# Performance work log

Hardware: AMD Instinct MI355X
Metric: run time of the kernel (lower is better)

The kernel has to match this reference:

```python
import jax, jax.numpy as jnp
import numpy as np

N_STATIONS = 276
CONTEXT_LEN = 384  # args.context_len * 2
TARGET_LEN = 96
BATCH = 4096


def setup_inputs() -> dict:
    key = jax.random.key(0)
    k1, k2, k3, k4, k5, k6 = jax.random.split(key, 6)
    z = jax.random.normal(k1, (BATCH, CONTEXT_LEN), dtype=jnp.float32)
    stations = jax.random.randint(k2, (BATCH,), 0, N_STATIONS, dtype=jnp.int64)
    # per-station Linear params (nn.Linear(context_len, target_len) x n_stations)
    lim = 1.0 / np.sqrt(CONTEXT_LEN)
    W = jax.random.uniform(k3, (N_STATIONS, TARGET_LEN, CONTEXT_LEN), jnp.float32, -lim, lim)
    b = jax.random.uniform(k4, (N_STATIONS, TARGET_LEN), jnp.float32, -lim, lim)
    loc = jax.random.normal(k5, (N_STATIONS,), dtype=jnp.float32)
    scale = jax.random.uniform(k6, (N_STATIONS,), jnp.float32, 0.5, 2.0)
    return {"z": z, "stations": stations, "W": W, "b": b, "loc": loc, "scale": scale}


def reference(z, stations, W, b, loc, scale):
    # norm: (z - loc[i]) / scale[i]
    loc_i = loc[stations][:, None]      # (bs, 1)
    scale_i = scale[stations][:, None]  # (bs, 1)
    zn = (z - loc_i) / scale_i          # (bs, context_len)
    # per-sample station-specific Linear: batched GEMV via gathered weights
    out = jnp.einsum("boi,bi->bo", W[stations], zn) + b[stations]  # (bs, target_len)
    # denorm then softplus
    out = out * scale_i + loc_i
    return jax.nn.softplus(out)
```

## Files before the change

kernel.cpp:

```cpp
#include <hip/hip_runtime.h>
#include <hip/hip_bf16.h>
#include <math.h>

#define N_STATIONS 276
#define CTX 384
#define TGT 96
#define BATCH 4096
#define NT_MAX 532
#define NPANEL 12

typedef __attribute__((ext_vector_type(8))) short bf16x8;
typedef __attribute__((ext_vector_type(4))) float f32x4;
typedef const void __attribute__((address_space(1)))* gas_ptr;
typedef void __attribute__((address_space(3)))* las_ptr;

__device__ __forceinline__ short f2bf(float f) {
    return (short)__builtin_bit_cast(unsigned short, __float2bfloat16(f));
}
__device__ __forceinline__ float bf2f(short h) {
    unsigned u = ((unsigned)(unsigned short)h) << 16;
    return __builtin_bit_cast(float, u);
}
__device__ __forceinline__ void cvt_hilo(float4 a, float4 b, bf16x8& hi, bf16x8& lo) {
    float f[8] = {a.x, a.y, a.z, a.w, b.x, b.y, b.z, b.w};
#pragma unroll
    for (int i = 0; i < 8; ++i) {
        short h = f2bf(f[i]);
        hi[i] = h;
        lo[i] = f2bf(f[i] - bf2f(h));
    }
}
__device__ __forceinline__ bf16x8 cvt_norm(float4 a, float4 b, float inv, float nb) {
    float f[8] = {a.x, a.y, a.z, a.w, b.x, b.y, b.z, b.w};
    bf16x8 r;
#pragma unroll
    for (int i = 0; i < 8; ++i) r[i] = f2bf(fmaf(f[i], inv, nb));
    return r;
}

__global__ __launch_bounds__(1024) void build_lists(
    const int* __restrict__ stations, int* __restrict__ ws)
{
    __shared__ int cnt[N_STATIONS], cnt2[N_STATIONS];
    __shared__ int poff[N_STATIONS + 1], tpoff[N_STATIONS + 1];
    const int tid = threadIdx.x;
    for (int i = tid; i < N_STATIONS; i += 1024) { cnt[i] = 0; cnt2[i] = 0; }
    __syncthreads();
    for (int b = tid; b < BATCH; b += 1024) atomicAdd(&cnt[stations[b]], 1);
    __syncthreads();
    if (tid < 64) {
        int run = 0, trun = 0;
        for (int base = 0; base < N_STATIONS; base += 64) {
            const int i = base + tid;
            int c  = (i < N_STATIONS) ? cnt[i] : 0;
            int v  = c, tv = (c + 15) >> 4;
#pragma unroll
            for (int off = 1; off < 64; off <<= 1) {
                int u  = __shfl_up(v, off, 64);
                int tu = __shfl_up(tv, off, 64);
                if (tid >= off) { v += u; tv += tu; }
            }
            if (i < N_STATIONS) { poff[i + 1] = run + v; tpoff[i + 1] = trun + tv; }
            run  += __shfl(v, 63, 64);
            trun += __shfl(tv, 63, 64);
        }
        if (tid == 0) { poff[0] = 0; tpoff[0] = 0; }
    }
    __syncthreads();
    int* order = ws + 1024;
    for (int b = tid; b < BATCH; b += 1024) {
        int s = stations[b];
        int p = atomicAdd(&cnt2[s], 1);
        order[poff[s] + p] = b;
    }
    for (int i = tid; i < N_STATIONS; i += 1024) {
        int n = (cnt[i] + 15) >> 4, base = tpoff[i];
        for (int t = 0; t < n; ++t) ws[1 + base + t] = (i << 16) | t;
    }
    if (tid <= N_STATIONS) ws[5120 + tid] = poff[tid];
    if (tid == 0) ws[0] = tpoff[N_STATIONS];
}

__global__ __launch_bounds__(384, 1) void nlinear_panels(
    const float* __restrict__ z,
    const float* __restrict__ W,
    const float* __restrict__ bias,
    const float* __restrict__ loc,
    const float* __restrict__ scale,
    const int*   __restrict__ ws,
    float*       __restrict__ out)
{
    __shared__ float lds[2][TGT * 32];

    const int ntiles = ws[0];
    const int b0 = blockIdx.x;
    const int xcd = b0 & 7, pos = b0 >> 3;
    const int b = (xcd < 4 ? xcd * 67 : 268 + (xcd - 4) * 66) + pos;
    if (b >= ntiles) return;

    const int* tiles   = ws + 1;
    const int* order   = ws + 1024;
    const int* offsets = ws + 5120;

    const int pk = tiles[b];
    const int s  = pk >> 16;
    const int tt = pk & 0xFFFF;
    const int start = offsets[s];
    const int m     = offsets[s + 1] - start;

    const int tidx = threadIdx.x;
    const int l  = tidx & 63;
    const int wv = tidx >> 6;
    const int lr = l & 15;
    const int kh = (l >> 4) * 8;

    const float lc = loc[s], sc = scale[s];
    const float inv = 1.0f / sc, nb = -lc * inv;

    int j = tt * 16 + lr; if (j > m - 1) j = m - 1;
    const float* zr = z + (size_t)order[start + j] * CTX + kh;
    bf16x8 af[NPANEL];
#pragma unroll
    for (int kk = 0; kk < NPANEL; ++kk) {
        float4 a0 = *(const float4*)(zr + kk * 32);
        float4 a1 = *(const float4*)(zr + kk * 32 + 4);
        af[kk] = cvt_norm(a0, a1, inv, nb);
    }

    const int rbase = (l >> 4) * 4;
    int oid[4]; bool ok[4];
#pragma unroll
    for (int r = 0; r < 4; ++r) {
        int jj = tt * 16 + rbase + r;
        ok[r]  = (jj < m);
        oid[r] = order[start + (ok[r] ? jj : 0)];
    }
    const float bv = bias[(size_t)s * TGT + wv * 16 + lr];

    const float* Wb = W + (size_t)s * TGT * CTX;
    const float* src[2]; int ldsoff[2];
#pragma unroll
    for (int jc = 0; jc < 2; ++jc) {
        const int q   = (wv * 2 + jc) * 64 + l;
        const int rw  = q >> 3;
        const int scn = (q & 7) ^ (rw & 7);
        src[jc]    = Wb + (size_t)rw * CTX + scn * 4;
        ldsoff[jc] = (wv * 2 + jc) * 256;
    }

#pragma unroll
    for (int jc = 0; jc < 2; ++jc)
        __builtin_amdgcn_global_load_lds((gas_ptr)(src[jc]), (las_ptr)&lds[0][ldsoff[jc]], 16, 0, 0);
#pragma unroll
    for (int jc = 0; jc < 2; ++jc)
        __builtin_amdgcn_global_load_lds((gas_ptr)(src[jc] + 32), (las_ptr)&lds[1][ldsoff[jc]], 16, 0, 0);
    __syncthreads();

    const int row = wv * 16 + lr;
    const int c0  = kh >> 2;
    const int s0  = row * 8 + (c0 ^ (row & 7));
    const int s1  = row * 8 + ((c0 + 1) ^ (row & 7));

    f32x4 ah = {0.f,0.f,0.f,0.f}, al = {0.f,0.f,0.f,0.f};
    for (int kk = 0; kk < NPANEL; ++kk) {
        const float* buf = lds[kk & 1];
        float4 a0 = *(const float4*)(buf + s0 * 4);
        float4 a1 = *(const float4*)(buf + s1 * 4);
        bf16x8 bhi, blo;
        cvt_hilo(a0, a1, bhi, blo);
        ah = __builtin_amdgcn_mfma_f32_16x16x32_bf16(af[kk], bhi, ah, 0, 0, 0);
        al = __builtin_amdgcn_mfma_f32_16x16x32_bf16(af[kk], blo, al, 0, 0, 0);
        __syncthreads();
        if (kk < NPANEL - 2) {
#pragma unroll
            for (int jc = 0; jc < 2; ++jc)
                __builtin_amdgcn_global_load_lds((gas_ptr)(src[jc] + (kk + 2) * 32),
                                                 (las_ptr)&lds[kk & 1][ldsoff[jc]], 16, 0, 0);
        }
    }

#pragma unroll
    for (int r = 0; r < 4; ++r) {
        if (ok[r]) {
            float v = (ah[r] + al[r] + bv) * sc + lc;
            out[(size_t)oid[r] * TGT + wv * 16 + lr] =
                fmaxf(v, 0.f) + log1pf(expf(-fabsf(v)));
        }
    }
}

extern "C" void kernel_launch(void* const* d_in, const int* in_sizes, int n_in,
                              void* d_out, int out_size, void* d_ws, size_t ws_size,
                              hipStream_t stream) {
    const float* z        = (const float*)d_in[0];
    const int*   stations = (const int*)  d_in[1];
    const float* W        = (const float*)d_in[2];
    const float* bias     = (const float*)d_in[3];
    const float* loc      = (const float*)d_in[4];
    const float* scale    = (const float*)d_in[5];
    float* out = (float*)d_out;
    int* ws = (int*)d_ws;

    build_lists<<<1, 1024, 0, stream>>>(stations, ws);
    nlinear_panels<<<NT_MAX, 384, 0, stream>>>(z, W, bias, loc, scale, ws, out);
}
```

Measured before the change: 36.09 us.

## Load station weights directly into registers in one burst instead of LDS pipeline

Replaces the double-buffered LDS staging of the weight panels (global_load_lds with barriers per K-step) with each lane issuing all 24 float4 weight loads straight into VGPRs up front, alongside the z loads. The MFMA loop then runs fully unrolled with no LDS traffic or __syncthreads. This aims to maximize memory-level parallelism and remove barrier stalls. The cost is much higher register pressure (96 extra VGPRs) and uncoalesced-per-row global reads that each lane fetches separately.

```diff
diff --git a/kernel.cpp b/kernel.cpp
--- a/kernel.cpp
+++ b/kernel.cpp
@@ -7,12 +7,9 @@
 #define TGT 96
 #define BATCH 4096
 #define NT_MAX 532
-#define NPANEL 12
 
 typedef __attribute__((ext_vector_type(8))) short bf16x8;
 typedef __attribute__((ext_vector_type(4))) float f32x4;
-typedef const void __attribute__((address_space(1)))* gas_ptr;
-typedef void __attribute__((address_space(3)))* las_ptr;
 
 __device__ __forceinline__ short f2bf(float f) {
     return (short)__builtin_bit_cast(unsigned short, __float2bfloat16(f));
@@ -81,7 +78,7 @@
     if (tid == 0) ws[0] = tpoff[N_STATIONS];
 }
 
-__global__ __launch_bounds__(384, 1) void nlinear_panels(
+__global__ __launch_bounds__(384, 1) void nlinear_wburst(
     const float* __restrict__ z,
     const float* __restrict__ W,
     const float* __restrict__ bias,
@@ -90,8 +87,6 @@
     const int*   __restrict__ ws,
     float*       __restrict__ out)
 {
-    __shared__ float lds[2][TGT * 32];
-
     const int ntiles = ws[0];
     const int b0 = blockIdx.x;
     const int xcd = b0 & 7, pos = b0 >> 3;
@@ -117,73 +112,47 @@
     const float lc = loc[s], sc = scale[s];
     const float inv = 1.0f / sc, nb = -lc * inv;
 
+    const float* wr = W + ((size_t)s * TGT + wv * 16 + lr) * CTX + kh;
+    float4 wl[24];
+#pragma unroll
+    for (int kk = 0; kk < 12; ++kk) {
+        wl[2 * kk]     = *(const float4*)(wr + kk * 32);
+        wl[2 * kk + 1] = *(const float4*)(wr + kk * 32 + 4);
+    }
+
     int j = tt * 16 + lr; if (j > m - 1) j = m - 1;
     const float* zr = z + (size_t)order[start + j] * CTX + kh;
-    bf16x8 af[NPANEL];
+    bf16x8 af[12];
 #pragma unroll
-    for (int kk = 0; kk < NPANEL; ++kk) {
+    for (int kk = 0; kk < 12; ++kk) {
         float4 a0 = *(const float4*)(zr + kk * 32);
         float4 a1 = *(const float4*)(zr + kk * 32 + 4);
         af[kk] = cvt_norm(a0, a1, inv, nb);
     }
 
+#pragma unroll
+    for (int i = 0; i < 24; ++i)
+        asm volatile("" : "+v"(wl[i].x), "+v"(wl[i].y), "+v"(wl[i].z), "+v"(wl[i].w));
+
+    f32x4 ah = {0.f, 0.f, 0.f, 0.f};
+    f32x4 al = {0.f, 0.f, 0.f, 0.f};
+#pragma unroll
+    for (int kk = 0; kk < 12; ++kk) {
+        bf16x8 bhi, blo;
+        cvt_hilo(wl[2 * kk], wl[2 * kk + 1], bhi, blo);
+        ah = __builtin_amdgcn_mfma_f32_16x16x32_bf16(af[kk], bhi, ah, 0, 0, 0);
+        al = __builtin_amdgcn_mfma_f32_16x16x32_bf16(af[kk], blo, al, 0, 0, 0);
+    }
+
+    const float bv = bias[(size_t)s * TGT + wv * 16 + lr];
     const int rbase = (l >> 4) * 4;
-    int oid[4]; bool ok[4];
 #pragma unroll
     for (int r = 0; r < 4; ++r) {
-        int jj = tt * 16 + rbase + r;
-        ok[r]  = (jj < m);
-        oid[r] = order[start + (ok[r] ? jj : 0)];
-    }
-    const float bv = bias[(size_t)s * TGT + wv * 16 + lr];
-
-    const float* Wb = W + (size_t)s * TGT * CTX;
-    const float* src[2]; int ldsoff[2];
-#pragma unroll
-    for (int jc = 0; jc < 2; ++jc) {
-        const int q   = (wv * 2 + jc) * 64 + l;
-        const int rw  = q >> 3;
-        const int scn = (q & 7) ^ (rw & 7);
-        src[jc]    = Wb + (size_t)rw * CTX + scn * 4;
-        ldsoff[jc] = (wv * 2 + jc) * 256;
-    }
-
-#pragma unroll
-    for (int jc = 0; jc < 2; ++jc)
-        __builtin_amdgcn_global_load_lds((gas_ptr)(src[jc]), (las_ptr)&lds[0][ldsoff[jc]], 16, 0, 0);
-#pragma unroll
-    for (int jc = 0; jc < 2; ++jc)
-        __builtin_amdgcn_global_load_lds((gas_ptr)(src[jc] + 32), (las_ptr)&lds[1][ldsoff[jc]], 16, 0, 0);
-    __syncthreads();
-
-    const int row = wv * 16 + lr;
-    const int c0  = kh >> 2;
-    const int s0  = row * 8 + (c0 ^ (row & 7));
-    const int s1  = row * 8 + ((c0 + 1) ^ (row & 7));
-
-    f32x4 ah = {0.f,0.f,0.f,0.f}, al = {0.f,0.f,0.f,0.f};
-    for (int kk = 0; kk < NPANEL; ++kk) {
-        const float* buf = lds[kk & 1];
-        float4 a0 = *(const float4*)(buf + s0 * 4);
-        float4 a1 = *(const float4*)(buf + s1 * 4);
-        bf16x8 bhi, blo;
-        cvt_hilo(a0, a1, bhi, blo);
-        ah = __builtin_amdgcn_mfma_f32_16x16x32_bf16(af[kk], bhi, ah, 0, 0, 0);
-        al = __builtin_amdgcn_mfma_f32_16x16x32_bf16(af[kk], blo, al, 0, 0, 0);
-        __syncthreads();
-        if (kk < NPANEL - 2) {
-#pragma unroll
-            for (int jc = 0; jc < 2; ++jc)
-                __builtin_amdgcn_global_load_lds((gas_ptr)(src[jc] + (kk + 2) * 32),
-                                                 (las_ptr)&lds[kk & 1][ldsoff[jc]], 16, 0, 0);
-        }
-    }
-
-#pragma unroll
-    for (int r = 0; r < 4; ++r) {
-        if (ok[r]) {
+        const int jj = tt * 16 + rbase + r;
+        if (jj < m) {
+            const int oid = order[start + jj];
             float v = (ah[r] + al[r] + bv) * sc + lc;
-            out[(size_t)oid[r] * TGT + wv * 16 + lr] =
+            out[(size_t)oid * TGT + wv * 16 + lr] =
                 fmaxf(v, 0.f) + log1pf(expf(-fabsf(v)));
         }
     }
@@ -202,5 +171,5 @@
     int* ws = (int*)d_ws;
 
     build_lists<<<1, 1024, 0, stream>>>(stations, ws);
-    nlinear_panels<<<NT_MAX, 384, 0, stream>>>(z, W, bias, loc, scale, ws, out);
+    nlinear_wburst<<<NT_MAX, 384, 0, stream>>>(z, W, bias, loc, scale, ws, out);
 }
```

Result: slower. 43.92 us (+21.7%).
